# Kernel optimization log

Hardware: AMD Instinct MI355X
Metric: run time of the kernel (lower is better)

Reference implementation:

```python
import jax, jax.numpy as jnp
import numpy as np

B, SQ, SKV, D, H = 2, 2048, 2048, 1024, 16
HD = D // H  # 64


def _lecun(key, shape):
    fan_in = int(np.prod(shape[:-2])) if len(shape) > 2 else shape[0]
    # DenseGeneral kernels: qkv kernels are (D, H, HD) with fan_in=D;
    # proj kernel is (H, HD, D) with fan_in=H*HD.
    return jax.random.normal(key, shape, jnp.float32) / np.sqrt(fan_in).astype(np.float32)


def setup_inputs() -> dict:
    key = jax.random.key(0)
    ks = jax.random.split(key, 6)
    inputs_q = jax.random.normal(ks[0], (B, SQ, D), jnp.float32)
    inputs_kv = jax.random.normal(ks[1], (B, SKV, D), jnp.float32)
    Wq = jax.random.normal(ks[2], (D, H, HD), jnp.float32) / np.float32(np.sqrt(D))
    Wk = jax.random.normal(ks[3], (D, H, HD), jnp.float32) / np.float32(np.sqrt(D))
    Wv = jax.random.normal(ks[4], (D, H, HD), jnp.float32) / np.float32(np.sqrt(D))
    Wo = jax.random.normal(ks[5], (H, HD, D), jnp.float32) / np.float32(np.sqrt(H * HD))
    bq = jnp.zeros((H, HD), jnp.float32)
    bk = jnp.zeros((H, HD), jnp.float32)
    bv = jnp.zeros((H, HD), jnp.float32)
    bo = jnp.zeros((D,), jnp.float32)
    return dict(inputs_q=inputs_q, inputs_kv=inputs_kv, Wq=Wq, bq=bq,
                Wk=Wk, bk=bk, Wv=Wv, bv=bv, Wo=Wo, bo=bo)


def reference(inputs_q, inputs_kv, Wq, bq, Wk, bk, Wv, bv, Wo, bo):
    # QKV projections: [B,S,D] x [D,H,HD] -> [B,S,H,HD]
    q = jnp.einsum('bsd,dhf->bshf', inputs_q, Wq) + bq
    k = jnp.einsum('bsd,dhf->bshf', inputs_kv, Wk) + bk
    v = jnp.einsum('bsd,dhf->bshf', inputs_kv, Wv) + bv
    # scores [B,H,SQ,SKV], scaled by sqrt(head_dim), softmax over keys
    attn = jnp.einsum('bqhf,bkhf->bhqk', q, k) / np.float32(np.sqrt(HD))
    attn = jax.nn.softmax(attn, axis=-1)
    ctx = jnp.einsum('bhqk,bkhf->bqhf', attn, v)
    out = jnp.einsum('bqhf,hfd->bqd', ctx, Wo) + bo
    return out, attn
```

## Files before the change

### kernel.cpp

```cpp
#include <hip/hip_runtime.h>
#include <math.h>

#define B_ 2
#define S_ 2048
#define D_ 1024
#define H_ 16
#define HD_ 64
#define BH_ (B_*H_)
#define OUT0_ (B_*S_*D_)

typedef __attribute__((ext_vector_type(8))) short bf16x8;
typedef __attribute__((ext_vector_type(4))) float floatx4;
typedef __attribute__((ext_vector_type(8))) short short8_t;
typedef __attribute__((ext_vector_type(4))) short short4_t;

static __device__ __forceinline__ short f2bf(float x) {
    union { float f; unsigned u; } c; c.f = x;
    unsigned r = (c.u + 0x7fffu + ((c.u >> 16) & 1u)) >> 16;
    return (short)r;
}

__global__ __launch_bounds__(256) void cvt_kernel(
    const float* __restrict__ src, short* __restrict__ dst, int n4)
{
    int i = blockIdx.x * 256 + threadIdx.x;
    if (i >= n4) return;
    float4 v = *(const float4*)&src[(size_t)i * 4];
    short4_t o;
    o.x = f2bf(v.x); o.y = f2bf(v.y); o.z = f2bf(v.z); o.w = f2bf(v.w);
    *(short4_t*)&dst[(size_t)i * 4] = o;
}

__global__ __launch_bounds__(256) void cvtT_kernel(
    const float* __restrict__ src, short* __restrict__ dst)
{
    __shared__ short Tl[64 * 72];
    const int t = threadIdx.x;
    const int r0 = blockIdx.y * 64;
    const int c0 = blockIdx.x * 64;
    {
        const int r = t >> 2, cq = t & 3;
#pragma unroll
        for (int u = 0; u < 4; ++u) {
            float4 v = *(const float4*)&src[(size_t)(r0 + r) * 1024 + c0 + cq * 16 + u * 4];
            Tl[r * 72 + cq * 16 + u * 4 + 0] = f2bf(v.x);
            Tl[r * 72 + cq * 16 + u * 4 + 1] = f2bf(v.y);
            Tl[r * 72 + cq * 16 + u * 4 + 2] = f2bf(v.z);
            Tl[r * 72 + cq * 16 + u * 4 + 3] = f2bf(v.w);
        }
    }
    __syncthreads();
    {
        const int c = t >> 2, rq = t & 3;
        short tmp[16];
#pragma unroll
        for (int u = 0; u < 16; ++u) tmp[u] = Tl[(rq * 16 + u) * 72 + c];
        *(short8_t*)&dst[(size_t)(c0 + c) * 1024 + r0 + rq * 16] = *(short8_t*)&tmp[0];
        *(short8_t*)&dst[(size_t)(c0 + c) * 1024 + r0 + rq * 16 + 8] = *(short8_t*)&tmp[8];
    }
}

__global__ __launch_bounds__(256) void transpose_v_kernel(
    const short* __restrict__ Vh, short* __restrict__ Vt)
{
    __shared__ short Tl[64 * 72];
    const int t = threadIdx.x;
    const int bh = blockIdx.y;
    const int s0 = blockIdx.x * 64;
    {
        const int r = t >> 2, cq = t & 3;
        *(short8_t*)&Tl[r * 72 + cq * 16] =
            *(const short8_t*)&Vh[((size_t)bh * S_ + s0 + r) * HD_ + cq * 16];
        *(short8_t*)&Tl[r * 72 + cq * 16 + 8] =
            *(const short8_t*)&Vh[((size_t)bh * S_ + s0 + r) * HD_ + cq * 16 + 8];
    }
    __syncthreads();
    {
        const int f = t >> 2, rq = t & 3;
        short tmp[16];
#pragma unroll
        for (int u = 0; u < 16; ++u) tmp[u] = Tl[(rq * 16 + u) * 72 + f];
        *(short8_t*)&Vt[((size_t)bh * HD_ + f) * S_ + s0 + rq * 16] = *(short8_t*)&tmp[0];
        *(short8_t*)&Vt[((size_t)bh * HD_ + f) * S_ + s0 + rq * 16 + 8] = *(short8_t*)&tmp[8];
    }
}

__global__ __launch_bounds__(256) void gemm_bf16_kernel(
    const short* __restrict__ A, const short* __restrict__ Bt,
    const float* __restrict__ bias, void* __restrict__ Y, int mode)
{
    __shared__ short Al[128 * 40];
    __shared__ short Bl[128 * 40];
    const int t = threadIdx.x;
    const int w = t >> 6, lane = t & 63;
    const int quad = lane >> 4, l16 = lane & 15;
    const int wm = w >> 1, wn = w & 1;
    const int m0 = blockIdx.y * 128;
    const int n0 = blockIdx.x * 128;

    floatx4 acc[4][4] = {};

    const int r = t >> 1, h = t & 1;
    for (int k0 = 0; k0 < 1024; k0 += 32) {
        *(short8_t*)&Al[r * 40 + h * 16] =
            *(const short8_t*)&A[(size_t)(m0 + r) * 1024 + k0 + h * 16];
        *(short8_t*)&Al[r * 40 + h * 16 + 8] =
            *(const short8_t*)&A[(size_t)(m0 + r) * 1024 + k0 + h * 16 + 8];
        *(short8_t*)&Bl[r * 40 + h * 16] =
            *(const short8_t*)&Bt[(size_t)(n0 + r) * 1024 + k0 + h * 16];
        *(short8_t*)&Bl[r * 40 + h * 16 + 8] =
            *(const short8_t*)&Bt[(size_t)(n0 + r) * 1024 + k0 + h * 16 + 8];
        __syncthreads();
        bf16x8 a[4], b[4];
#pragma unroll
        for (int i = 0; i < 4; ++i)
            a[i] = *(const bf16x8*)&Al[(wm * 64 + i * 16 + l16) * 40 + quad * 8];
#pragma unroll
        for (int j = 0; j < 4; ++j)
            b[j] = *(const bf16x8*)&Bl[(wn * 64 + j * 16 + l16) * 40 + quad * 8];
#pragma unroll
        for (int i = 0; i < 4; ++i)
#pragma unroll
            for (int j = 0; j < 4; ++j)
                acc[i][j] = __builtin_amdgcn_mfma_f32_16x16x32_bf16(a[i], b[j], acc[i][j], 0, 0, 0);
        __syncthreads();
    }

#pragma unroll
    for (int i = 0; i < 4; ++i) {
#pragma unroll
        for (int j = 0; j < 4; ++j) {
            const int col = n0 + wn * 64 + j * 16 + l16;
            const float bcol = bias[col];
#pragma unroll
            for (int rr = 0; rr < 4; ++rr) {
                const int row = m0 + wm * 64 + i * 16 + quad * 4 + rr;
                const float v = acc[i][j][rr] + bcol;
                if (mode == 0) {
                    ((float*)Y)[(size_t)row * 1024 + col] = v;
                } else {
                    const int b = row >> 11, s = row & 2047;
                    const int hh = col >> 6, f = col & 63;
                    ((short*)Y)[(((size_t)(b * H_ + hh) * S_) + s) * HD_ + f] = f2bf(v);
                }
            }
        }
    }
}

__global__ __launch_bounds__(256) void stats_kernel(
    const short* __restrict__ Qh, const short* __restrict__ Kh,
    float* __restrict__ M, float* __restrict__ LI)
{
    __shared__ short Kl[128 * 72];
    __shared__ float sm[2][128];
    __shared__ float sl[2][128];
    const int t = threadIdx.x;
    const int w = t >> 6, lane = t & 63;
    const int quad = lane >> 4, l16 = lane & 15;
    const int wm = w >> 1, wn = w & 1;
    const int bh = blockIdx.y;
    const int q0 = blockIdx.x * 128;

    bf16x8 qf[4][2];
#pragma unroll
    for (int i = 0; i < 4; ++i)
#pragma unroll
        for (int ks = 0; ks < 2; ++ks)
            qf[i][ks] = *(const bf16x8*)&Qh[((size_t)bh * S_ + q0 + wm * 64 + i * 16 + l16) * HD_ + ks * 32 + quad * 8];

    float m_p[16], l_p[16];
#pragma unroll
    for (int x = 0; x < 16; ++x) { m_p[x] = -1e30f; l_p[x] = 0.0f; }

    for (int c0 = 0; c0 < S_; c0 += 128) {
        {
            const int r = t >> 1, h2 = t & 1;
            const short* ksrc = &Kh[((size_t)bh * S_ + c0 + r) * HD_ + h2 * 32];
#pragma unroll
            for (int u = 0; u < 4; ++u)
                *(short8_t*)&Kl[r * 72 + h2 * 32 + u * 8] = *(const short8_t*)&ksrc[u * 8];
        }
        __syncthreads();
        floatx4 acc[4][4] = {};
#pragma unroll
        for (int ks = 0; ks < 2; ++ks) {
            bf16x8 b[4];
#pragma unroll
            for (int j = 0; j < 4; ++j)
                b[j] = *(const bf16x8*)&Kl[(wn * 64 + j * 16 + l16) * 72 + ks * 32 + quad * 8];
#pragma unroll
            for (int i = 0; i < 4; ++i)
#pragma unroll
                for (int j = 0; j < 4; ++j)
                    acc[i][j] = __builtin_amdgcn_mfma_f32_16x16x32_bf16(qf[i][ks], b[j], acc[i][j], 0, 0, 0);
        }
        __syncthreads();
#pragma unroll
        for (int i = 0; i < 4; ++i)
#pragma unroll
            for (int rr = 0; rr < 4; ++rr) {
                const int idx = i * 4 + rr;
                const float s0 = acc[i][0][rr] * 0.125f, s1 = acc[i][1][rr] * 0.125f;
                const float s2 = acc[i][2][rr] * 0.125f, s3 = acc[i][3][rr] * 0.125f;
                const float tm = fmaxf(fmaxf(s0, s1), fmaxf(s2, s3));
                const float mn = fmaxf(m_p[idx], tm);
                l_p[idx] = l_p[idx] * __expf(m_p[idx] - mn)
                         + __expf(s0 - mn) + __expf(s1 - mn)
                         + __expf(s2 - mn) + __expf(s3 - mn);
                m_p[idx] = mn;
            }
    }
#pragma unroll
    for (int idx = 0; idx < 16; ++idx) {
#pragma unroll
        for (int off = 1; off < 16; off <<= 1) {
            const float mo = __shfl_xor(m_p[idx], off);
            const float lo = __shfl_xor(l_p[idx], off);
            const float mn = fmaxf(m_p[idx], mo);
            l_p[idx] = l_p[idx] * __expf(m_p[idx] - mn) + lo * __expf(mo - mn);
            m_p[idx] = mn;
        }
    }
    if (l16 == 0) {
#pragma unroll
        for (int i = 0; i < 4; ++i)
#pragma unroll
            for (int rr = 0; rr < 4; ++rr) {
                const int row = wm * 64 + i * 16 + quad * 4 + rr;
                sm[wn][row] = m_p[i * 4 + rr];
                sl[wn][row] = l_p[i * 4 + rr];
            }
    }
    __syncthreads();
    if (t < 128) {
        const float m0v = sm[0][t], m1v = sm[1][t];
        const float mn = fmaxf(m0v, m1v);
        const float l = sl[0][t] * __expf(m0v - mn) + sl[1][t] * __expf(m1v - mn);
        M[(size_t)bh * S_ + q0 + t] = mn;
        LI[(size_t)bh * S_ + q0 + t] = 1.0f / l;
    }
}

#define PPAD 136
#define VPAD 136
__global__ __launch_bounds__(256) void fused_attn_kernel(
    const short* __restrict__ Qh, const short* __restrict__ Kh,
    const short* __restrict__ Vt, const float* __restrict__ M,
    const float* __restrict__ LI, float* __restrict__ attn,
    short* __restrict__ CTX)
{
    __shared__ short Kl[128 * 72];
    __shared__ short Pl[128 * PPAD];
    __shared__ short Vl[64 * VPAD];
    const int t = threadIdx.x;
    const int w = t >> 6, lane = t & 63;
    const int quad = lane >> 4, l16 = lane & 15;
    const int wm = w >> 1, wn = w & 1;
    const int bh = blockIdx.y;
    const int q0 = blockIdx.x * 128;
    const int b = bh >> 4, hh = bh & 15;

    bf16x8 qf[4][2];
#pragma unroll
    for (int i = 0; i < 4; ++i)
#pragma unroll
        for (int ks = 0; ks < 2; ++ks)
            qf[i][ks] = *(const bf16x8*)&Qh[((size_t)bh * S_ + q0 + wm * 64 + i * 16 + l16) * HD_ + ks * 32 + quad * 8];

    float m_r[16], li_r[16];
#pragma unroll
    for (int i = 0; i < 4; ++i)
#pragma unroll
        for (int rr = 0; rr < 4; ++rr) {
            const int row = q0 + wm * 64 + i * 16 + quad * 4 + rr;
            m_r[i * 4 + rr]  = M[(size_t)bh * S_ + row];
            li_r[i * 4 + rr] = LI[(size_t)bh * S_ + row];
        }

    floatx4 acc2[2][4] = {};

    for (int c0 = 0; c0 < S_; c0 += 128) {
        {
            const int r = t >> 1, h2 = t & 1;
            const short* ksrc = &Kh[((size_t)bh * S_ + c0 + r) * HD_ + h2 * 32];
#pragma unroll
            for (int u = 0; u < 4; ++u)
                *(short8_t*)&Kl[r * 72 + h2 * 32 + u * 8] = *(const short8_t*)&ksrc[u * 8];
        }
        {
            const int f = t >> 2, part = t & 3;
            const short* vsrc = &Vt[((size_t)bh * HD_ + f) * S_ + c0 + part * 32];
#pragma unroll
            for (int u = 0; u < 4; ++u)
                *(short8_t*)&Vl[f * VPAD + part * 32 + u * 8] = *(const short8_t*)&vsrc[u * 8];
        }
        __syncthreads();

        floatx4 acc[4][4] = {};
#pragma unroll
        for (int ks = 0; ks < 2; ++ks) {
            bf16x8 bfr[4];
#pragma unroll
            for (int j = 0; j < 4; ++j)
                bfr[j] = *(const bf16x8*)&Kl[(wn * 64 + j * 16 + l16) * 72 + ks * 32 + quad * 8];
#pragma unroll
            for (int i = 0; i < 4; ++i)
#pragma unroll
                for (int j = 0; j < 4; ++j)
                    acc[i][j] = __builtin_amdgcn_mfma_f32_16x16x32_bf16(qf[i][ks], bfr[j], acc[i][j], 0, 0, 0);
        }

#pragma unroll
        for (int i = 0; i < 4; ++i)
#pragma unroll
            for (int rr = 0; rr < 4; ++rr) {
                const int idx = i * 4 + rr;
                const int row = wm * 64 + i * 16 + quad * 4 + rr;
                float* adst = &attn[((size_t)bh * S_ + q0 + row) * S_ + c0 + wn * 64 + l16];
                short* pdst = &Pl[row * PPAD + wn * 64 + l16];
#pragma unroll
                for (int j = 0; j < 4; ++j) {
                    const float p = __expf(acc[i][j][rr] * 0.125f - m_r[idx]) * li_r[idx];
                    __builtin_nontemporal_store(p, &adst[j * 16]);
                    pdst[j * 16] = f2bf(p);
                }
            }
        __syncthreads();

#pragma unroll
        for (int ks2 = 0; ks2 < 4; ++ks2) {
            bf16x8 a2[2], bv[4];
#pragma unroll
            for (int i = 0; i < 2; ++i)
                a2[i] = *(const bf16x8*)&Pl[(w * 32 + i * 16 + l16) * PPAD + ks2 * 32 + quad * 8];
#pragma unroll
            for (int j = 0; j < 4; ++j)
                bv[j] = *(const bf16x8*)&Vl[(j * 16 + l16) * VPAD + ks2 * 32 + quad * 8];
#pragma unroll
            for (int i = 0; i < 2; ++i)
#pragma unroll
                for (int j = 0; j < 4; ++j)
                    acc2[i][j] = __builtin_amdgcn_mfma_f32_16x16x32_bf16(a2[i], bv[j], acc2[i][j], 0, 0, 0);
        }
        __syncthreads();
    }

#pragma unroll
    for (int i = 0; i < 2; ++i)
#pragma unroll
        for (int j = 0; j < 4; ++j) {
            const int col = j * 16 + l16;
#pragma unroll
            for (int rr = 0; rr < 4; ++rr) {
                const int s = q0 + w * 32 + i * 16 + quad * 4 + rr;
                CTX[((size_t)(b * S_ + s)) * 1024 + hh * 64 + col] = f2bf(acc2[i][j][rr]);
            }
        }
}

extern "C" void kernel_launch(void* const* d_in, const int* in_sizes, int n_in,
                              void* d_out, int out_size, void* d_ws, size_t ws_size,
                              hipStream_t stream)
{
    const float* Xq  = (const float*)d_in[0];
    const float* Xkv = (const float*)d_in[1];
    const float* Wq  = (const float*)d_in[2];
    const float* bq  = (const float*)d_in[3];
    const float* Wk  = (const float*)d_in[4];
    const float* bk  = (const float*)d_in[5];
    const float* Wv  = (const float*)d_in[6];
    const float* bv  = (const float*)d_in[7];
    const float* Wo  = (const float*)d_in[8];
    const float* bo  = (const float*)d_in[9];

    float* out  = (float*)d_out;
    float* attn = out + OUT0_;

    short* ws = (short*)d_ws;
    short* XQB  = ws;
    short* XKVB = ws + 4194304;
    short* WQT  = ws + 8388608;
    short* WKT  = ws + 9437184;
    short* WVT  = ws + 10485760;
    short* WOT  = ws + 11534336;
    short* QH   = ws + 12582912;
    short* KH   = ws + 16777216;
    short* VH   = ws + 20971520;
    short* VT   = ws + 25165824;
    short* CTXB = ws + 29360128;
    float* Mst  = (float*)ws;
    float* LIst = (float*)(ws + 131072);

    dim3 blk(256);

    cvt_kernel<<<dim3(4096), blk, 0, stream>>>(Xq,  XQB,  1048576);
    cvt_kernel<<<dim3(4096), blk, 0, stream>>>(Xkv, XKVB, 1048576);
    cvtT_kernel<<<dim3(16, 16), blk, 0, stream>>>(Wq, WQT);
    cvtT_kernel<<<dim3(16, 16), blk, 0, stream>>>(Wk, WKT);
    cvtT_kernel<<<dim3(16, 16), blk, 0, stream>>>(Wv, WVT);
    cvtT_kernel<<<dim3(16, 16), blk, 0, stream>>>(Wo, WOT);

    gemm_bf16_kernel<<<dim3(8, 32), blk, 0, stream>>>(XQB,  WQT, bq, QH, 1);
    gemm_bf16_kernel<<<dim3(8, 32), blk, 0, stream>>>(XKVB, WKT, bk, KH, 1);
    gemm_bf16_kernel<<<dim3(8, 32), blk, 0, stream>>>(XKVB, WVT, bv, VH, 1);

    transpose_v_kernel<<<dim3(32, 32), blk, 0, stream>>>(VH, VT);

    stats_kernel<<<dim3(16, 32), blk, 0, stream>>>(QH, KH, Mst, LIst);
    fused_attn_kernel<<<dim3(16, 32), blk, 0, stream>>>(QH, KH, VT, Mst, LIst, attn, CTXB);

    gemm_bf16_kernel<<<dim3(8, 32), blk, 0, stream>>>(CTXB, WOT, bo, out, 0);

    (void)in_sizes; (void)n_in; (void)out_size; (void)ws_size;
}
```

Before: 859.4 us.

## Use direct-to-LDS loads, XCD-aware block remap, and transposed QK^T MFMA

The GEMM kernel now stages A and B tiles with global_load_lds straight into unpadded LDS instead of going through registers, and remaps workgroup IDs so neighbouring tiles land on the same XCD for L2 reuse. The stats and attention kernels apply the same XCD-aware remap and swap the MFMA operand order so each lane holds four consecutive key columns for a single query row. This turns the fp32 attention-probability writes into 16-byte vector nontemporal stores, packs the bf16 P tile as short4 writes, and cuts the per-lane softmax state from 16 rows to 4. The unpadded GEMM LDS layout risks more bank conflicts on the fragment reads.

```diff
diff --git a/kernel.cpp b/kernel.cpp
--- a/kernel.cpp
+++ b/kernel.cpp
@@ -18,6 +18,12 @@
     union { float f; unsigned u; } c; c.f = x;
     unsigned r = (c.u + 0x7fffu + ((c.u >> 16) & 1u)) >> 16;
     return (short)r;
+}
+
+static __device__ __forceinline__ void gload16(const short* g, short* l) {
+    __builtin_amdgcn_global_load_lds(
+        (const __attribute__((address_space(1))) unsigned int*)g,
+        (__attribute__((address_space(3))) unsigned int*)l, 16, 0, 0);
 }
 
 __global__ __launch_bounds__(256) void cvt_kernel(
@@ -89,35 +95,38 @@
     const short* __restrict__ A, const short* __restrict__ Bt,
     const float* __restrict__ bias, void* __restrict__ Y, int mode)
 {
-    __shared__ short Al[128 * 40];
-    __shared__ short Bl[128 * 40];
+    __shared__ __attribute__((aligned(16))) short Al[128 * 32];
+    __shared__ __attribute__((aligned(16))) short Bl[128 * 32];
     const int t = threadIdx.x;
     const int w = t >> 6, lane = t & 63;
     const int quad = lane >> 4, l16 = lane & 15;
     const int wm = w >> 1, wn = w & 1;
-    const int m0 = blockIdx.y * 128;
-    const int n0 = blockIdx.x * 128;
+
+    const int nwg = gridDim.x * gridDim.y;
+    const int cpx = nwg >> 3;
+    const int id0 = blockIdx.y * gridDim.x + blockIdx.x;
+    const int lid = (id0 & 7) * cpx + (id0 >> 3);
+    const int n0 = (lid % gridDim.x) * 128;
+    const int m0 = (lid / gridDim.x) * 128;
 
     floatx4 acc[4][4] = {};
 
-    const int r = t >> 1, h = t & 1;
+    const int r_a = lane >> 2;
+    const int kc  = (lane & 3) * 8;
+
     for (int k0 = 0; k0 < 1024; k0 += 32) {
-        *(short8_t*)&Al[r * 40 + h * 16] =
-            *(const short8_t*)&A[(size_t)(m0 + r) * 1024 + k0 + h * 16];
-        *(short8_t*)&Al[r * 40 + h * 16 + 8] =
-            *(const short8_t*)&A[(size_t)(m0 + r) * 1024 + k0 + h * 16 + 8];
-        *(short8_t*)&Bl[r * 40 + h * 16] =
-            *(const short8_t*)&Bt[(size_t)(n0 + r) * 1024 + k0 + h * 16];
-        *(short8_t*)&Bl[r * 40 + h * 16 + 8] =
-            *(const short8_t*)&Bt[(size_t)(n0 + r) * 1024 + k0 + h * 16 + 8];
+        gload16(&A[(size_t)(m0 + w * 16 + r_a) * 1024 + k0 + kc],      &Al[w * 512]);
+        gload16(&A[(size_t)(m0 + 64 + w * 16 + r_a) * 1024 + k0 + kc], &Al[2048 + w * 512]);
+        gload16(&Bt[(size_t)(n0 + w * 16 + r_a) * 1024 + k0 + kc],      &Bl[w * 512]);
+        gload16(&Bt[(size_t)(n0 + 64 + w * 16 + r_a) * 1024 + k0 + kc], &Bl[2048 + w * 512]);
         __syncthreads();
         bf16x8 a[4], b[4];
 #pragma unroll
         for (int i = 0; i < 4; ++i)
-            a[i] = *(const bf16x8*)&Al[(wm * 64 + i * 16 + l16) * 40 + quad * 8];
+            a[i] = *(const bf16x8*)&Al[(wm * 64 + i * 16 + l16) * 32 + quad * 8];
 #pragma unroll
         for (int j = 0; j < 4; ++j)
-            b[j] = *(const bf16x8*)&Bl[(wn * 64 + j * 16 + l16) * 40 + quad * 8];
+            b[j] = *(const bf16x8*)&Bl[(wn * 64 + j * 16 + l16) * 32 + quad * 8];
 #pragma unroll
         for (int i = 0; i < 4; ++i)
 #pragma unroll
@@ -139,9 +148,9 @@
                 if (mode == 0) {
                     ((float*)Y)[(size_t)row * 1024 + col] = v;
                 } else {
-                    const int b = row >> 11, s = row & 2047;
+                    const int b2 = row >> 11, s = row & 2047;
                     const int hh = col >> 6, f = col & 63;
-                    ((short*)Y)[(((size_t)(b * H_ + hh) * S_) + s) * HD_ + f] = f2bf(v);
+                    ((short*)Y)[(((size_t)(b2 * H_ + hh) * S_) + s) * HD_ + f] = f2bf(v);
                 }
             }
         }
@@ -159,8 +168,11 @@
     const int w = t >> 6, lane = t & 63;
     const int quad = lane >> 4, l16 = lane & 15;
     const int wm = w >> 1, wn = w & 1;
-    const int bh = blockIdx.y;
-    const int q0 = blockIdx.x * 128;
+
+    const int id0 = blockIdx.y * gridDim.x + blockIdx.x;
+    const int lid = (id0 & 7) * 64 + (id0 >> 3);
+    const int bh = lid >> 4;
+    const int q0 = (lid & 15) * 128;
 
     bf16x8 qf[4][2];
 #pragma unroll
@@ -169,9 +181,9 @@
         for (int ks = 0; ks < 2; ++ks)
             qf[i][ks] = *(const bf16x8*)&Qh[((size_t)bh * S_ + q0 + wm * 64 + i * 16 + l16) * HD_ + ks * 32 + quad * 8];
 
-    float m_p[16], l_p[16];
-#pragma unroll
-    for (int x = 0; x < 16; ++x) { m_p[x] = -1e30f; l_p[x] = 0.0f; }
+    float m_p[4], l_p[4];
+#pragma unroll
+    for (int x = 0; x < 4; ++x) { m_p[x] = -1e30f; l_p[x] = 0.0f; }
 
     for (int c0 = 0; c0 < S_; c0 += 128) {
         {
@@ -185,52 +197,52 @@
         floatx4 acc[4][4] = {};
 #pragma unroll
         for (int ks = 0; ks < 2; ++ks) {
-            bf16x8 b[4];
+            bf16x8 kf[4];
 #pragma unroll
             for (int j = 0; j < 4; ++j)
-                b[j] = *(const bf16x8*)&Kl[(wn * 64 + j * 16 + l16) * 72 + ks * 32 + quad * 8];
+                kf[j] = *(const bf16x8*)&Kl[(wn * 64 + j * 16 + l16) * 72 + ks * 32 + quad * 8];
 #pragma unroll
             for (int i = 0; i < 4; ++i)
 #pragma unroll
                 for (int j = 0; j < 4; ++j)
-                    acc[i][j] = __builtin_amdgcn_mfma_f32_16x16x32_bf16(qf[i][ks], b[j], acc[i][j], 0, 0, 0);
-        }
-        __syncthreads();
-#pragma unroll
-        for (int i = 0; i < 4; ++i)
-#pragma unroll
-            for (int rr = 0; rr < 4; ++rr) {
-                const int idx = i * 4 + rr;
-                const float s0 = acc[i][0][rr] * 0.125f, s1 = acc[i][1][rr] * 0.125f;
-                const float s2 = acc[i][2][rr] * 0.125f, s3 = acc[i][3][rr] * 0.125f;
-                const float tm = fmaxf(fmaxf(s0, s1), fmaxf(s2, s3));
-                const float mn = fmaxf(m_p[idx], tm);
-                l_p[idx] = l_p[idx] * __expf(m_p[idx] - mn)
-                         + __expf(s0 - mn) + __expf(s1 - mn)
-                         + __expf(s2 - mn) + __expf(s3 - mn);
-                m_p[idx] = mn;
-            }
-    }
-#pragma unroll
-    for (int idx = 0; idx < 16; ++idx) {
-#pragma unroll
-        for (int off = 1; off < 16; off <<= 1) {
-            const float mo = __shfl_xor(m_p[idx], off);
-            const float lo = __shfl_xor(l_p[idx], off);
-            const float mn = fmaxf(m_p[idx], mo);
-            l_p[idx] = l_p[idx] * __expf(m_p[idx] - mn) + lo * __expf(mo - mn);
-            m_p[idx] = mn;
-        }
-    }
-    if (l16 == 0) {
-#pragma unroll
-        for (int i = 0; i < 4; ++i)
-#pragma unroll
-            for (int rr = 0; rr < 4; ++rr) {
-                const int row = wm * 64 + i * 16 + quad * 4 + rr;
-                sm[wn][row] = m_p[i * 4 + rr];
-                sl[wn][row] = l_p[i * 4 + rr];
-            }
+                    acc[i][j] = __builtin_amdgcn_mfma_f32_16x16x32_bf16(kf[j], qf[i][ks], acc[i][j], 0, 0, 0);
+        }
+        __syncthreads();
+#pragma unroll
+        for (int i = 0; i < 4; ++i) {
+            float s[16];
+#pragma unroll
+            for (int j = 0; j < 4; ++j)
+#pragma unroll
+                for (int rr = 0; rr < 4; ++rr) s[j * 4 + rr] = acc[i][j][rr] * 0.125f;
+            float tm = s[0];
+#pragma unroll
+            for (int x = 1; x < 16; ++x) tm = fmaxf(tm, s[x]);
+            const float mn = fmaxf(m_p[i], tm);
+            float add = 0.0f;
+#pragma unroll
+            for (int x = 0; x < 16; ++x) add += __expf(s[x] - mn);
+            l_p[i] = l_p[i] * __expf(m_p[i] - mn) + add;
+            m_p[i] = mn;
+        }
+    }
+#pragma unroll
+    for (int i = 0; i < 4; ++i) {
+#pragma unroll
+        for (int off = 16; off < 64; off <<= 1) {
+            const float mo = __shfl_xor(m_p[i], off);
+            const float lo = __shfl_xor(l_p[i], off);
+            const float mn = fmaxf(m_p[i], mo);
+            l_p[i] = l_p[i] * __expf(m_p[i] - mn) + lo * __expf(mo - mn);
+            m_p[i] = mn;
+        }
+    }
+    if (quad == 0) {
+#pragma unroll
+        for (int i = 0; i < 4; ++i) {
+            sm[wn][wm * 64 + i * 16 + l16] = m_p[i];
+            sl[wn][wm * 64 + i * 16 + l16] = l_p[i];
+        }
     }
     __syncthreads();
     if (t < 128) {
@@ -257,8 +269,11 @@
     const int w = t >> 6, lane = t & 63;
     const int quad = lane >> 4, l16 = lane & 15;
     const int wm = w >> 1, wn = w & 1;
-    const int bh = blockIdx.y;
-    const int q0 = blockIdx.x * 128;
+
+    const int id0 = blockIdx.y * gridDim.x + blockIdx.x;
+    const int lid = (id0 & 7) * 64 + (id0 >> 3);
+    const int bh = lid >> 4;
+    const int q0 = (lid & 15) * 128;
     const int b = bh >> 4, hh = bh & 15;
 
     bf16x8 qf[4][2];
@@ -268,15 +283,13 @@
         for (int ks = 0; ks < 2; ++ks)
             qf[i][ks] = *(const bf16x8*)&Qh[((size_t)bh * S_ + q0 + wm * 64 + i * 16 + l16) * HD_ + ks * 32 + quad * 8];
 
-    float m_r[16], li_r[16];
-#pragma unroll
-    for (int i = 0; i < 4; ++i)
-#pragma unroll
-        for (int rr = 0; rr < 4; ++rr) {
-            const int row = q0 + wm * 64 + i * 16 + quad * 4 + rr;
-            m_r[i * 4 + rr]  = M[(size_t)bh * S_ + row];
-            li_r[i * 4 + rr] = LI[(size_t)bh * S_ + row];
-        }
+    float m_r[4], li_r[4];
+#pragma unroll
+    for (int i = 0; i < 4; ++i) {
+        const int row = q0 + wm * 64 + i * 16 + l16;
+        m_r[i]  = M[(size_t)bh * S_ + row];
+        li_r[i] = LI[(size_t)bh * S_ + row];
+    }
 
     floatx4 acc2[2][4] = {};
 
@@ -300,32 +313,35 @@
         floatx4 acc[4][4] = {};
 #pragma unroll
         for (int ks = 0; ks < 2; ++ks) {
-            bf16x8 bfr[4];
+            bf16x8 kf[4];
 #pragma unroll
             for (int j = 0; j < 4; ++j)
-                bfr[j] = *(const bf16x8*)&Kl[(wn * 64 + j * 16 + l16) * 72 + ks * 32 + quad * 8];
+                kf[j] = *(const bf16x8*)&Kl[(wn * 64 + j * 16 + l16) * 72 + ks * 32 + quad * 8];
 #pragma unroll
             for (int i = 0; i < 4; ++i)
 #pragma unroll
                 for (int j = 0; j < 4; ++j)
-                    acc[i][j] = __builtin_amdgcn_mfma_f32_16x16x32_bf16(qf[i][ks], bfr[j], acc[i][j], 0, 0, 0);
-        }
-
-#pragma unroll
-        for (int i = 0; i < 4; ++i)
-#pragma unroll
-            for (int rr = 0; rr < 4; ++rr) {
-                const int idx = i * 4 + rr;
-                const int row = wm * 64 + i * 16 + quad * 4 + rr;
-                float* adst = &attn[((size_t)bh * S_ + q0 + row) * S_ + c0 + wn * 64 + l16];
-                short* pdst = &Pl[row * PPAD + wn * 64 + l16];
-#pragma unroll
-                for (int j = 0; j < 4; ++j) {
-                    const float p = __expf(acc[i][j][rr] * 0.125f - m_r[idx]) * li_r[idx];
-                    __builtin_nontemporal_store(p, &adst[j * 16]);
-                    pdst[j * 16] = f2bf(p);
+                    acc[i][j] = __builtin_amdgcn_mfma_f32_16x16x32_bf16(kf[j], qf[i][ks], acc[i][j], 0, 0, 0);
+        }
+
+#pragma unroll
+        for (int i = 0; i < 4; ++i) {
+            const int qrow = wm * 64 + i * 16 + l16;
+#pragma unroll
+            for (int j = 0; j < 4; ++j) {
+                const int col = wn * 64 + j * 16 + quad * 4;
+                floatx4 pv;
+                short4_t ps;
+#pragma unroll
+                for (int rr = 0; rr < 4; ++rr) {
+                    const float p = __expf(fmaf(acc[i][j][rr], 0.125f, -m_r[i])) * li_r[i];
+                    pv[rr] = p; ps[rr] = f2bf(p);
                 }
+                __builtin_nontemporal_store(pv,
+                    (floatx4*)&attn[((size_t)bh * S_ + q0 + qrow) * S_ + c0 + col]);
+                *(short4_t*)&Pl[qrow * PPAD + col] = ps;
             }
+        }
         __syncthreads();
 
 #pragma unroll
```

Result: faster. 831.5 us (-3.2%).
